# Performance work log

Measured on AMD Instinct MI355X. Metric: run time of the kernel, lower is better.

Reference implementation:

```python
import jax, jax.numpy as jnp
import numpy as np

IN_CHANNELS = 512
NUM_HEADS = 8
HEAD_CH = IN_CHANNELS // NUM_HEADS


def setup_inputs() -> dict:
    key = jax.random.key(0)
    k0, k1, k2, k3, k4 = jax.random.split(key, 5)
    B, C, H, W = 4, IN_CHANNELS, 128, 128
    x = jax.random.normal(k0, (B, C, H, W), dtype=jnp.float32)
    # 1x1 Conv2d weights == per-pixel linear layers over channels
    s_in = 1.0 / np.sqrt(C)
    Wqkv = jax.random.uniform(k1, (3 * C, C), dtype=jnp.float32, minval=-s_in, maxval=s_in)
    bqkv = jax.random.uniform(k2, (3 * C,), dtype=jnp.float32, minval=-s_in, maxval=s_in)
    Wout = jax.random.uniform(k3, (C, C), dtype=jnp.float32, minval=-s_in, maxval=s_in)
    bout = jax.random.uniform(k4, (C,), dtype=jnp.float32, minval=-s_in, maxval=s_in)
    return {"x": x, "Wqkv": Wqkv, "bqkv": bqkv, "Wout": Wout, "bout": bout}


def _axial_attention(x, Wqkv, bqkv, Wout, bout):
    B, C, H, W = x.shape
    nh, d = NUM_HEADS, HEAD_CH
    scale = 1.0 / jnp.sqrt(jnp.asarray(d, dtype=x.dtype))

    # 1x1 conv qkv projection: [B, 3C, H, W]
    qkv = jnp.einsum('bchw,oc->bohw', x, Wqkv) + bqkv[None, :, None, None]
    q, k, v = jnp.split(qkv, 3, axis=1)
    # [B, nh, d, H, W]
    q = q.reshape(B, nh, d, H, W)
    k = k.reshape(B, nh, d, H, W)
    v = v.reshape(B, nh, d, H, W)

    # Row attention: for each row h, attend across width (w over u)
    scores_row = jnp.einsum('bndhw,bndhu->bnhwu', q, k) * scale  # [B,nh,H,W,W]
    probs_row = jax.nn.softmax(scores_row, axis=-1)
    out_row = jnp.einsum('bnhwu,bndhu->bndhw', probs_row, v)  # [B,nh,d,H,W]

    # Column attention: for each column w, attend across height (h over g)
    scores_col = jnp.einsum('bndhw,bndgw->bnwhg', q, k) * scale  # [B,nh,W,H,H]
    probs_col = jax.nn.softmax(scores_col, axis=-1)
    out_col = jnp.einsum('bnwhg,bndgw->bndhw', probs_col, v)  # [B,nh,d,H,W]

    out = (out_row + out_col).reshape(B, C, H, W)
    # 1x1 conv output projection
    return jnp.einsum('bchw,oc->bohw', out, Wout) + bout[None, :, None, None]


def reference(x, Wqkv, bqkv, Wout, bout):
    return _axial_attention(x, Wqkv, bqkv, Wout, bout)
```

## Files before the change

### kernel.cpp

```cpp
#include <hip/hip_runtime.h>

#define DI __device__ __forceinline__

typedef __attribute__((ext_vector_type(4))) float f32x4;
typedef __attribute__((ext_vector_type(8))) short s16x8;
typedef __attribute__((ext_vector_type(4))) short s16x4;
typedef unsigned short u16;

#define AS_G(p) ((const __attribute__((address_space(1))) void*)(p))
#define AS_L(p) ((__attribute__((address_space(3))) void*)(p))

DI short f2bf(float f) {
  union { float f; unsigned u; } v; v.f = f;
  unsigned r = v.u + 0x7FFFu + ((v.u >> 16) & 1u);
  return (short)(r >> 16);
}
DI float bf2f(short h) {
  union { unsigned u; float f; } v; v.u = ((unsigned)(u16)h) << 16; return v.f;
}

#define MFMA(a, b, c) __builtin_amdgcn_mfma_f32_16x16x32_bf16((a), (b), (c), 0, 0, 0)

__global__ void cast_weights_kernel(const float* __restrict__ wqkv, u16* __restrict__ wqkv_bf,
                                    const float* __restrict__ wout, u16* __restrict__ wout_bf) {
  const int n1 = 1536 * 512 / 4, n2 = 512 * 512 / 4;
  for (int c = blockIdx.x * blockDim.x + threadIdx.x; c < n1 + n2; c += gridDim.x * blockDim.x) {
    const float4* src; u16* dst; int idx;
    if (c < n1) { src = (const float4*)wqkv; dst = wqkv_bf; idx = c; }
    else        { src = (const float4*)wout; dst = wout_bf; idx = c - n1; }
    float4 v = src[idx];
    s16x4 o;
    o[0] = f2bf(v.x); o[1] = f2bf(v.y); o[2] = f2bf(v.z); o[3] = f2bf(v.w);
    *(s16x4*)(dst + (long)idx * 4) = o;
  }
}

template<bool IN_F32>
__global__ __launch_bounds__(256)
void transpose_kernel(const void* __restrict__ in, u16* __restrict__ out,
                      int in_rstride, int out_rstride, long plane_in, long plane_out) {
  __shared__ __align__(16) u16 t[64][72];
  const int tid = threadIdx.x;
  const long bi = (long)blockIdx.z * plane_in;
  const long bo = (long)blockIdx.z * plane_out;
  const int r0 = blockIdx.y * 64, c0 = blockIdx.x * 64;
#pragma unroll
  for (int i = 0; i < 4; ++i) {
    int c = tid + i * 256;
    int row = c >> 4, c4 = c & 15;
    s16x4 pk;
    if (IN_F32) {
      const float4 v = *(const float4*)((const float*)in + bi + (long)(r0 + row) * in_rstride + c0 + c4 * 4);
      pk[0] = f2bf(v.x); pk[1] = f2bf(v.y); pk[2] = f2bf(v.z); pk[3] = f2bf(v.w);
    } else {
      pk = *(const s16x4*)((const u16*)in + bi + (long)(r0 + row) * in_rstride + c0 + c4 * 4);
    }
    *(s16x4*)&t[row][c4 * 4] = pk;
  }
  __syncthreads();
#pragma unroll
  for (int i = 0; i < 2; ++i) {
    int c = tid + i * 256;
    int orow = c >> 3, u = c & 7;
    s16x8 pk;
#pragma unroll
    for (int j = 0; j < 8; ++j) pk[j] = (short)t[u * 8 + j][orow];
    *(s16x8*)(out + bo + (long)(c0 + orow) * out_rstride + r0 + u * 8) = pk;
  }
}

template<int EPI>
__global__ __launch_bounds__(256, 2)
void gemm_kernel(const u16* __restrict__ A, const u16* __restrict__ B,
                 const float* __restrict__ bias,
                 u16* __restrict__ out_qk, u16* __restrict__ out_v,
                 float* __restrict__ out_f) {
  __shared__ __align__(16) u16 sAB[2][16384];
  const int tid = threadIdx.x;
  const int lane = tid & 63, wid = tid >> 6;
  const int l15 = lane & 15, g4 = lane >> 4;
  const int wr = wid >> 1, wc = wid & 1;
  const int m0 = blockIdx.y * 128, n0 = blockIdx.x * 128;
  const int z = blockIdx.z;
  const u16* Bp = B + (long)z * 8388608;

  f32x4 acc[4][4];
#pragma unroll
  for (int i = 0; i < 4; ++i)
#pragma unroll
    for (int j = 0; j < 4; ++j) { f32x4 z4 = {0.f, 0.f, 0.f, 0.f}; acc[i][j] = z4; }

  const int srow = wid * 32 + (lane >> 3);
  const int su = lane & 7;
  auto stage = [&](int kt, int buf) {
    u16* As = sAB[buf];
    u16* Bs = sAB[buf] + 8192;
#pragma unroll
    for (int i = 0; i < 4; ++i) {
      int row = srow + i * 8;
      int ksw = (su ^ (row & 7)) * 8;
      __builtin_amdgcn_global_load_lds(AS_G(A + (long)(m0 + row) * 512 + kt * 64 + ksw),
                                       AS_L(As + wid * 2048 + i * 512), 16, 0, 0);
    }
#pragma unroll
    for (int i = 0; i < 4; ++i) {
      int row = srow + i * 8;
      int ksw = (su ^ (row & 7)) * 8;
      __builtin_amdgcn_global_load_lds(AS_G(Bp + (long)(n0 + row) * 512 + kt * 64 + ksw),
                                       AS_L(Bs + wid * 2048 + i * 512), 16, 0, 0);
    }
  };

  stage(0, 0);
  __syncthreads();
  int cur = 0;
  for (int kt = 0; kt < 8; ++kt) {
    if (kt < 7) stage(kt + 1, cur ^ 1);
    const u16* As = sAB[cur];
    const u16* Bs = sAB[cur] + 8192;
#pragma unroll
    for (int ks = 0; ks < 2; ++ks) {
      s16x8 af[4], bfr[4];
#pragma unroll
      for (int mi = 0; mi < 4; ++mi) {
        int row = (wr * 4 + mi) * 16 + l15;
        af[mi] = *(const s16x8*)(As + row * 64 + (((ks * 4 + g4) ^ (row & 7)) * 8));
      }
#pragma unroll
      for (int ni = 0; ni < 4; ++ni) {
        int row = (wc * 4 + ni) * 16 + l15;
        bfr[ni] = *(const s16x8*)(Bs + row * 64 + (((ks * 4 + g4) ^ (row & 7)) * 8));
      }
#pragma unroll
      for (int mi = 0; mi < 4; ++mi)
#pragma unroll
        for (int ni = 0; ni < 4; ++ni)
          acc[mi][ni] = MFMA(af[mi], bfr[ni], acc[mi][ni]);
    }
    __syncthreads();
    cur ^= 1;
  }

  u16* tile = (u16*)sAB;
  float* tilef = (float*)sAB;

  if (EPI == 0) {
    u16* qk_b = out_qk + (long)z * 16777216;
    u16* v_b  = out_v + (long)z * 8388608;
    if (m0 < 1024) {
#pragma unroll
      for (int mi = 0; mi < 4; ++mi) {
        int ol = (wr * 4 + mi) * 16 + 4 * g4;
        int o0 = m0 + ol;
        float b0 = bias[o0], b1 = bias[o0 + 1], b2 = bias[o0 + 2], b3 = bias[o0 + 3];
#pragma unroll
        for (int ni = 0; ni < 4; ++ni) {
          int pl = (wc * 4 + ni) * 16 + l15;
          s16x4 pk;
          pk[0] = f2bf(acc[mi][ni][0] + b0);
          pk[1] = f2bf(acc[mi][ni][1] + b1);
          pk[2] = f2bf(acc[mi][ni][2] + b2);
          pk[3] = f2bf(acc[mi][ni][3] + b3);
          *(s16x4*)(tile + pl * 136 + ol) = pk;
        }
      }
      __syncthreads();
#pragma unroll
      for (int i = 0; i < 8; ++i) {
        int row = i * 16 + (tid >> 4);
        int c8 = (tid & 15) * 8;
        s16x8 vr = *(const s16x8*)(tile + row * 136 + c8);
        *(s16x8*)(qk_b + (long)(n0 + row) * 1024 + m0 + c8) = vr;
      }
    } else {
#pragma unroll
      for (int mi = 0; mi < 4; ++mi) {
        int cl = (wr * 4 + mi) * 16 + 4 * g4;
        int o0 = m0 + cl;
#pragma unroll
        for (int ni = 0; ni < 4; ++ni) {
          int pl = (wc * 4 + ni) * 16 + l15;
#pragma unroll
          for (int r = 0; r < 4; ++r)
            tile[(cl + r) * 136 + pl] = (u16)f2bf(acc[mi][ni][r] + bias[o0 + r]);
        }
      }
      __syncthreads();
#pragma unroll
      for (int i = 0; i < 8; ++i) {
        int row = i * 16 + (tid >> 4);
        int c8 = (tid & 15) * 8;
        s16x8 vr = *(const s16x8*)(tile + row * 136 + c8);
        *(s16x8*)(v_b + (long)(m0 - 1024 + row) * 16384 + n0 + c8) = vr;
      }
    }
  } else {
    float* of = out_f + (long)z * 8388608;
#pragma unroll
    for (int pass = 0; pass < 2; ++pass) {
      if (pass) __syncthreads();
#pragma unroll
      for (int mi2 = 0; mi2 < 2; ++mi2) {
        int mi = pass * 2 + mi2;
        int ol = mi2 * 16 + 4 * g4 + ((wr & 1) ? 64 : 0);
        (void)ol;
      }
      if (wr == pass) {
#pragma unroll
        for (int mi = 0; mi < 4; ++mi) {
          int ol = (wr * 4 + mi) * 16 + 4 * g4;
          int o0 = m0 + ol;
          float b0 = bias[o0], b1 = bias[o0 + 1], b2 = bias[o0 + 2], b3 = bias[o0 + 3];
          float bb[4] = {b0, b1, b2, b3};
#pragma unroll
          for (int ni = 0; ni < 4; ++ni) {
            int pl = (wc * 4 + ni) * 16 + l15;
#pragma unroll
            for (int r = 0; r < 4; ++r)
              tilef[(ol - pass * 64 + r) * 136 + pl] = acc[mi][ni][r] + bb[r];
          }
        }
      }
      __syncthreads();
#pragma unroll
      for (int i = 0; i < 8; ++i) {
        int row = i * 8 + (tid >> 5);
        int c4 = (tid & 31) * 4;
        f32x4 vr = *(const f32x4*)(tilef + row * 136 + c4);
        *(f32x4*)(of + (long)(m0 + pass * 64 + row) * 16384 + n0 + c4) = vr;
      }
    }
  }
}

template<int MODE>
__global__ __launch_bounds__(512, 2)
void attn_kernel(const u16* __restrict__ qk_t_g, const u16* __restrict__ vsrc_g,
                 u16* __restrict__ outp_g) {
  __shared__ __align__(16) u16 smem[24576];
  u16* qT = smem;
  u16* kT = smem + 8192;
  u16* vS = smem + 16384;
  u16* P  = smem;

  const int tid = threadIdx.x;
  const int lane = tid & 63, wid = tid >> 6;
  const int l15 = lane & 15, g4 = lane >> 4;
  const int b = blockIdx.x >> 10;
  const int gidx = blockIdx.x & 1023;
  const int n = gidx >> 7, pos = gidx & 127;

  const u16* qk_t = qk_t_g + (long)b * 16777216;
  const u16* vsrc = vsrc_g + (long)b * 8388608;
  u16* outp = outp_g + (long)b * 8388608;

  long q_base, q_rstride;
  if (MODE == 0) { q_base = (long)pos * 128 * 1024 + n * 64; q_rstride = 1024; }
  else           { q_base = (long)pos * 1024 + n * 64;       q_rstride = 128 * 1024; }
  const long v_base = (long)n * 64 * 16384 + (long)pos * 128;

#pragma unroll
  for (int j = 0; j < 6; ++j) {
    int t = wid + j * 8;
    if (t < 32) {
      int which = t >> 4;
      int tt = t & 15;
      int row = tt * 8 + (lane >> 3);
      int u = lane & 7;
      const u16* src = qk_t + q_base + which * 512 + (long)row * q_rstride + ((u ^ (row & 7)) * 8);
      __builtin_amdgcn_global_load_lds(AS_G(src), AS_L(smem + t * 512), 16, 0, 0);
    } else {
      int tt = t - 32;
      int row = tt * 4 + (lane >> 4);
      int u = lane & 15;
      const u16* src = vsrc + v_base + (long)row * 16384 + ((u ^ (row & 15)) * 8);
      __builtin_amdgcn_global_load_lds(AS_G(src), AS_L(smem + t * 512), 16, 0, 0);
    }
  }
  __syncthreads();

  f32x4 acc[8];
#pragma unroll
  for (int nt = 0; nt < 8; ++nt) { f32x4 zz = {0.f, 0.f, 0.f, 0.f}; acc[nt] = zz; }
  s16x8 aq[2];
  {
    int row = wid * 16 + l15;
#pragma unroll
    for (int ks = 0; ks < 2; ++ks)
      aq[ks] = *(const s16x8*)(qT + row * 64 + (((ks * 4 + g4) ^ (row & 7)) * 8));
  }
#pragma unroll
  for (int nt = 0; nt < 8; ++nt) {
    int rowk = nt * 16 + l15;
#pragma unroll
    for (int ks = 0; ks < 2; ++ks) {
      s16x8 bk = *(const s16x8*)(kT + rowk * 64 + (((ks * 4 + g4) ^ (rowk & 7)) * 8));
      acc[nt] = MFMA(aq[ks], bk, acc[nt]);
    }
  }

#pragma unroll
  for (int r = 0; r < 4; ++r) {
    float m = -1e30f;
#pragma unroll
    for (int nt = 0; nt < 8; ++nt) m = fmaxf(m, acc[nt][r]);
    m = fmaxf(m, __shfl_xor(m, 1));
    m = fmaxf(m, __shfl_xor(m, 2));
    m = fmaxf(m, __shfl_xor(m, 4));
    m = fmaxf(m, __shfl_xor(m, 8));
    float s = 0.f;
#pragma unroll
    for (int nt = 0; nt < 8; ++nt) {
      float e = __expf((acc[nt][r] - m) * 0.125f);
      acc[nt][r] = e; s += e;
    }
    s += __shfl_xor(s, 1); s += __shfl_xor(s, 2);
    s += __shfl_xor(s, 4); s += __shfl_xor(s, 8);
    float rinv = 1.0f / s;
#pragma unroll
    for (int nt = 0; nt < 8; ++nt) acc[nt][r] *= rinv;
  }
  __syncthreads();

#pragma unroll
  for (int nt = 0; nt < 8; ++nt) {
    int u = nt * 16 + l15;
#pragma unroll
    for (int r = 0; r < 4; ++r) {
      int w = wid * 16 + 4 * g4 + r;
      int ch = (u >> 3) ^ (w & 15);
      P[w * 128 + ch * 8 + (u & 7)] = (u16)f2bf(acc[nt][r]);
    }
  }
  __syncthreads();

  const int mw = wid >> 2, nw = wid & 3;
  f32x4 pacc[2][2];
#pragma unroll
  for (int mi = 0; mi < 2; ++mi)
#pragma unroll
    for (int ni = 0; ni < 2; ++ni) { f32x4 zz = {0.f, 0.f, 0.f, 0.f}; pacc[mi][ni] = zz; }
#pragma unroll
  for (int ks = 0; ks < 4; ++ks) {
    s16x8 av[2], bp[2];
#pragma unroll
    for (int mi = 0; mi < 2; ++mi) {
      int d = (mw * 2 + mi) * 16 + l15;
      av[mi] = *(const s16x8*)(vS + d * 128 + (((ks * 4 + g4) ^ (d & 15)) * 8));
    }
#pragma unroll
    for (int ni = 0; ni < 2; ++ni) {
      int w = (nw * 2 + ni) * 16 + l15;
      bp[ni] = *(const s16x8*)(P + w * 128 + (((ks * 4 + g4) ^ (w & 15)) * 8));
    }
#pragma unroll
    for (int mi = 0; mi < 2; ++mi)
#pragma unroll
      for (int ni = 0; ni < 2; ++ni)
        pacc[mi][ni] = MFMA(av[mi], bp[ni], pacc[mi][ni]);
  }

  long out_pbase, out_pstr;
  if (MODE == 0) { out_pbase = (long)pos * 128 * 512; out_pstr = 512; }
  else           { out_pbase = (long)pos * 512;       out_pstr = 128 * 512; }
#pragma unroll
  for (int mi = 0; mi < 2; ++mi) {
    int d0 = (mw * 2 + mi) * 16 + 4 * g4;
#pragma unroll
    for (int ni = 0; ni < 2; ++ni) {
      int nj = (nw * 2 + ni) * 16 + l15;
      long base = out_pbase + (long)nj * out_pstr + n * 64 + d0;
      if (MODE == 0) {
        s16x4 pk;
#pragma unroll
        for (int r = 0; r < 4; ++r) pk[r] = f2bf(pacc[mi][ni][r]);
        *(s16x4*)(outp + base) = pk;
      } else {
        s16x4 old = *(const s16x4*)(outp + base);
        s16x4 pk;
#pragma unroll
        for (int r = 0; r < 4; ++r) pk[r] = f2bf(bf2f(old[r]) + pacc[mi][ni][r]);
        *(s16x4*)(outp + base) = pk;
      }
    }
  }
}

extern "C" void kernel_launch(void* const* d_in, const int* in_sizes, int n_in,
                              void* d_out, int out_size, void* d_ws, size_t ws_size,
                              hipStream_t stream) {
  const float* x    = (const float*)d_in[0];
  const float* wqkv = (const float*)d_in[1];
  const float* bqkv = (const float*)d_in[2];
  const float* wout = (const float*)d_in[3];
  const float* bout = (const float*)d_in[4];
  float* out = (float*)d_out;

  char* ws = (char*)d_ws;
  size_t off = 0;
  auto alloc = [&](size_t bytes) { void* p = ws + off; off += (bytes + 255) & ~(size_t)255; return p; };
  u16* wqkv_bf = (u16*)alloc(1536L * 512 * 2);
  u16* wout_bf = (u16*)alloc(512L * 512 * 2);
  u16* xT      = (u16*)alloc(4L * 16384 * 512 * 2);
  u16* qk_t    = (u16*)alloc(4L * 16384 * 1024 * 2);
  u16* v_buf   = (u16*)alloc(4L * 512 * 16384 * 2);
  u16* vT      = (u16*)alloc(4L * 512 * 16384 * 2);
  u16* attn_T  = (u16*)alloc(4L * 16384 * 512 * 2);

  cast_weights_kernel<<<256, 256, 0, stream>>>(wqkv, wqkv_bf, wout, wout_bf);
  transpose_kernel<true><<<dim3(256, 8, 4), 256, 0, stream>>>(
      x, xT, 16384, 512, 512L * 16384, 16384L * 512);
  gemm_kernel<0><<<dim3(128, 12, 4), 256, 0, stream>>>(wqkv_bf, xT, bqkv, qk_t, v_buf, nullptr);
  transpose_kernel<false><<<dim3(2, 2, 2048), 256, 0, stream>>>(v_buf, vT, 128, 128, 16384, 16384);
  attn_kernel<0><<<dim3(4096), 512, 0, stream>>>(qk_t, v_buf, attn_T);
  attn_kernel<1><<<dim3(4096), 512, 0, stream>>>(qk_t, vT, attn_T);
  gemm_kernel<1><<<dim3(128, 4, 4), 256, 0, stream>>>(wout_bf, attn_T, bout, nullptr, nullptr, out);
}
```

Baseline: 387.0 us.

## Load GEMM A-operand fragments directly from global into registers, staging only B in LDS

The GEMM kernel no longer stages the weight (A) tile through shared memory. Each wave loads its MFMA A fragments straight from global memory into a double-buffered register array, prefetching the next k-tile, while B is still staged in LDS via global_load_lds. This halves LDS traffic and footprint per block, which may allow higher occupancy. The cost is more registers and uncoalesced 16-byte global loads for A that rely on cache hits, since A is shared across blocks.

```diff
diff --git a/kernel.cpp b/kernel.cpp
--- a/kernel.cpp
+++ b/kernel.cpp
@@ -75,7 +75,7 @@
                  const float* __restrict__ bias,
                  u16* __restrict__ out_qk, u16* __restrict__ out_v,
                  float* __restrict__ out_f) {
-  __shared__ __align__(16) u16 sAB[2][16384];
+  __shared__ __align__(16) u16 smem[17408];
   const int tid = threadIdx.x;
   const int lane = tid & 63, wid = tid >> 6;
   const int l15 = lane & 15, g4 = lane >> 4;
@@ -92,16 +92,8 @@
 
   const int srow = wid * 32 + (lane >> 3);
   const int su = lane & 7;
-  auto stage = [&](int kt, int buf) {
-    u16* As = sAB[buf];
-    u16* Bs = sAB[buf] + 8192;
-#pragma unroll
-    for (int i = 0; i < 4; ++i) {
-      int row = srow + i * 8;
-      int ksw = (su ^ (row & 7)) * 8;
-      __builtin_amdgcn_global_load_lds(AS_G(A + (long)(m0 + row) * 512 + kt * 64 + ksw),
-                                       AS_L(As + wid * 2048 + i * 512), 16, 0, 0);
-    }
+  auto stageB = [&](int kt, int buf) {
+    u16* Bs = smem + buf * 8192;
 #pragma unroll
     for (int i = 0; i < 4; ++i) {
       int row = srow + i * 8;
@@ -111,21 +103,34 @@
     }
   };
 
-  stage(0, 0);
+  s16x8 a_frag[2][4][2];
+
+#pragma unroll
+  for (int mi = 0; mi < 4; ++mi)
+#pragma unroll
+    for (int ks = 0; ks < 2; ++ks)
+      a_frag[0][mi][ks] = *(const s16x8*)(A + (long)(m0 + (wr * 4 + mi) * 16 + l15) * 512 +
+                                          (ks * 4 + g4) * 8);
+  stageB(0, 0);
   __syncthreads();
-  int cur = 0;
+
+#pragma unroll
   for (int kt = 0; kt < 8; ++kt) {
-    if (kt < 7) stage(kt + 1, cur ^ 1);
-    const u16* As = sAB[cur];
-    const u16* Bs = sAB[cur] + 8192;
+    const int cur = kt & 1;
+    if (kt < 7) {
+#pragma unroll
+      for (int mi = 0; mi < 4; ++mi)
+#pragma unroll
+        for (int ks = 0; ks < 2; ++ks)
+          a_frag[cur ^ 1][mi][ks] =
+              *(const s16x8*)(A + (long)(m0 + (wr * 4 + mi) * 16 + l15) * 512 +
+                              (kt + 1) * 64 + (ks * 4 + g4) * 8);
+      stageB(kt + 1, cur ^ 1);
+    }
+    const u16* Bs = smem + cur * 8192;
 #pragma unroll
     for (int ks = 0; ks < 2; ++ks) {
-      s16x8 af[4], bfr[4];
-#pragma unroll
-      for (int mi = 0; mi < 4; ++mi) {
-        int row = (wr * 4 + mi) * 16 + l15;
-        af[mi] = *(const s16x8*)(As + row * 64 + (((ks * 4 + g4) ^ (row & 7)) * 8));
-      }
+      s16x8 bfr[4];
 #pragma unroll
       for (int ni = 0; ni < 4; ++ni) {
         int row = (wc * 4 + ni) * 16 + l15;
@@ -135,14 +140,13 @@
       for (int mi = 0; mi < 4; ++mi)
 #pragma unroll
         for (int ni = 0; ni < 4; ++ni)
-          acc[mi][ni] = MFMA(af[mi], bfr[ni], acc[mi][ni]);
+          acc[mi][ni] = MFMA(a_frag[cur][mi][ks], bfr[ni], acc[mi][ni]);
     }
     __syncthreads();
-    cur ^= 1;
-  }
-
-  u16* tile = (u16*)sAB;
-  float* tilef = (float*)sAB;
+  }
+
+  u16* tile = smem;
+  float* tilef = (float*)smem;
 
   if (EPI == 0) {
     u16* qk_b = out_qk + (long)z * 16777216;
@@ -199,19 +203,12 @@
 #pragma unroll
     for (int pass = 0; pass < 2; ++pass) {
       if (pass) __syncthreads();
-#pragma unroll
-      for (int mi2 = 0; mi2 < 2; ++mi2) {
-        int mi = pass * 2 + mi2;
-        int ol = mi2 * 16 + 4 * g4 + ((wr & 1) ? 64 : 0);
-        (void)ol;
-      }
       if (wr == pass) {
 #pragma unroll
         for (int mi = 0; mi < 4; ++mi) {
           int ol = (wr * 4 + mi) * 16 + 4 * g4;
           int o0 = m0 + ol;
-          float b0 = bias[o0], b1 = bias[o0 + 1], b2 = bias[o0 + 2], b3 = bias[o0 + 3];
-          float bb[4] = {b0, b1, b2, b3};
+          float bb[4] = {bias[o0], bias[o0 + 1], bias[o0 + 2], bias[o0 + 3]};
 #pragma unroll
           for (int ni = 0; ni < 4; ++ni) {
             int pl = (wc * 4 + ni) * 16 + l15;
```

Measured after the change: 490.5 us. 26.7% more time.

## Enlarge GEMM tiles to 256x256 with 512-thread blocks

Applied to the files above, without the earlier changes.

Both projection GEMMs move from 128x128 tiles with 4 waves to 256x256 tiles with 8 waves, each wave computing a 128x64 sub-tile. Operand staging, the swizzled LDS layout and the multi-pass epilogues are rewritten to fit the larger 128KB shared buffer. The aim is more arithmetic per loaded byte and less global traffic for the A/B operands. In exchange, each block uses far more LDS and registers, which likely allows only one block per CU. The grid also shrinks to fewer blocks, so load balance across CUs may suffer.

```diff
diff --git a/kernel.cpp b/kernel.cpp
--- a/kernel.cpp
+++ b/kernel.cpp
@@ -70,163 +70,169 @@
 }
 
 template<int EPI>
-__global__ __launch_bounds__(256, 2)
+__global__ __launch_bounds__(512, 2)
 void gemm_kernel(const u16* __restrict__ A, const u16* __restrict__ B,
                  const float* __restrict__ bias,
                  u16* __restrict__ out_qk, u16* __restrict__ out_v,
                  float* __restrict__ out_f) {
-  __shared__ __align__(16) u16 sAB[2][16384];
+  __shared__ __align__(16) u16 smem[65536];
   const int tid = threadIdx.x;
   const int lane = tid & 63, wid = tid >> 6;
   const int l15 = lane & 15, g4 = lane >> 4;
-  const int wr = wid >> 1, wc = wid & 1;
-  const int m0 = blockIdx.y * 128, n0 = blockIdx.x * 128;
+  const int wr = wid >> 2, wc = wid & 3;
+  const int m0 = blockIdx.y * 256, n0 = blockIdx.x * 256;
   const int z = blockIdx.z;
   const u16* Bp = B + (long)z * 8388608;
 
-  f32x4 acc[4][4];
-#pragma unroll
-  for (int i = 0; i < 4; ++i)
+  f32x4 acc[8][4];
+#pragma unroll
+  for (int i = 0; i < 8; ++i)
 #pragma unroll
     for (int j = 0; j < 4; ++j) { f32x4 z4 = {0.f, 0.f, 0.f, 0.f}; acc[i][j] = z4; }
 
-  const int srow = wid * 32 + (lane >> 3);
-  const int su = lane & 7;
   auto stage = [&](int kt, int buf) {
-    u16* As = sAB[buf];
-    u16* Bs = sAB[buf] + 8192;
+    u16* As = smem + buf * 32768;
+    u16* Bs = As + 16384;
 #pragma unroll
     for (int i = 0; i < 4; ++i) {
-      int row = srow + i * 8;
-      int ksw = (su ^ (row & 7)) * 8;
-      __builtin_amdgcn_global_load_lds(AS_G(A + (long)(m0 + row) * 512 + kt * 64 + ksw),
-                                       AS_L(As + wid * 2048 + i * 512), 16, 0, 0);
+      int unit = tid + i * 512;
+      int row = unit >> 3;
+      int csw = ((unit & 7) ^ (row & 7)) * 8;
+      __builtin_amdgcn_global_load_lds(AS_G(A + (long)(m0 + row) * 512 + kt * 64 + csw),
+                                       AS_L(As + unit * 8), 16, 0, 0);
     }
 #pragma unroll
     for (int i = 0; i < 4; ++i) {
-      int row = srow + i * 8;
-      int ksw = (su ^ (row & 7)) * 8;
-      __builtin_amdgcn_global_load_lds(AS_G(Bp + (long)(n0 + row) * 512 + kt * 64 + ksw),
-                                       AS_L(Bs + wid * 2048 + i * 512), 16, 0, 0);
+      int unit = tid + i * 512;
+      int row = unit >> 3;
+      int csw = ((unit & 7) ^ (row & 7)) * 8;
+      __builtin_amdgcn_global_load_lds(AS_G(Bp + (long)(n0 + row) * 512 + kt * 64 + csw),
+                                       AS_L(Bs + unit * 8), 16, 0, 0);
     }
   };
 
   stage(0, 0);
   __syncthreads();
-  int cur = 0;
+#pragma unroll 2
   for (int kt = 0; kt < 8; ++kt) {
+    const int cur = kt & 1;
     if (kt < 7) stage(kt + 1, cur ^ 1);
-    const u16* As = sAB[cur];
-    const u16* Bs = sAB[cur] + 8192;
+    const u16* As = smem + cur * 32768;
+    const u16* Bs = As + 16384;
 #pragma unroll
     for (int ks = 0; ks < 2; ++ks) {
-      s16x8 af[4], bfr[4];
-#pragma unroll
-      for (int mi = 0; mi < 4; ++mi) {
-        int row = (wr * 4 + mi) * 16 + l15;
+      s16x8 af[8], bfr[4];
+#pragma unroll
+      for (int mi = 0; mi < 8; ++mi) {
+        int row = wr * 128 + mi * 16 + l15;
         af[mi] = *(const s16x8*)(As + row * 64 + (((ks * 4 + g4) ^ (row & 7)) * 8));
       }
 #pragma unroll
       for (int ni = 0; ni < 4; ++ni) {
-        int row = (wc * 4 + ni) * 16 + l15;
+        int row = wc * 64 + ni * 16 + l15;
         bfr[ni] = *(const s16x8*)(Bs + row * 64 + (((ks * 4 + g4) ^ (row & 7)) * 8));
       }
 #pragma unroll
-      for (int mi = 0; mi < 4; ++mi)
+      for (int mi = 0; mi < 8; ++mi)
 #pragma unroll
         for (int ni = 0; ni < 4; ++ni)
           acc[mi][ni] = MFMA(af[mi], bfr[ni], acc[mi][ni]);
     }
     __syncthreads();
-    cur ^= 1;
-  }
-
-  u16* tile = (u16*)sAB;
-  float* tilef = (float*)sAB;
+  }
+
+  u16* tile = smem;
+  float* tilef = (float*)smem;
 
   if (EPI == 0) {
     u16* qk_b = out_qk + (long)z * 16777216;
     u16* v_b  = out_v + (long)z * 8388608;
     if (m0 < 1024) {
 #pragma unroll
-      for (int mi = 0; mi < 4; ++mi) {
-        int ol = (wr * 4 + mi) * 16 + 4 * g4;
-        int o0 = m0 + ol;
-        float b0 = bias[o0], b1 = bias[o0 + 1], b2 = bias[o0 + 2], b3 = bias[o0 + 3];
-#pragma unroll
-        for (int ni = 0; ni < 4; ++ni) {
-          int pl = (wc * 4 + ni) * 16 + l15;
-          s16x4 pk;
-          pk[0] = f2bf(acc[mi][ni][0] + b0);
-          pk[1] = f2bf(acc[mi][ni][1] + b1);
-          pk[2] = f2bf(acc[mi][ni][2] + b2);
-          pk[3] = f2bf(acc[mi][ni][3] + b3);
-          *(s16x4*)(tile + pl * 136 + ol) = pk;
+      for (int pass = 0; pass < 2; ++pass) {
+        if (pass) __syncthreads();
+        if ((wc >> 1) == pass) {
+#pragma unroll
+          for (int mi = 0; mi < 8; ++mi) {
+            int ol = wr * 128 + mi * 16 + 4 * g4;
+            int o0 = m0 + ol;
+            float b0 = bias[o0], b1 = bias[o0 + 1], b2 = bias[o0 + 2], b3 = bias[o0 + 3];
+#pragma unroll
+            for (int ni = 0; ni < 4; ++ni) {
+              int pl = (wc & 1) * 64 + ni * 16 + l15;
+              s16x4 pk;
+              pk[0] = f2bf(acc[mi][ni][0] + b0);
+              pk[1] = f2bf(acc[mi][ni][1] + b1);
+              pk[2] = f2bf(acc[mi][ni][2] + b2);
+              pk[3] = f2bf(acc[mi][ni][3] + b3);
+              *(s16x4*)(tile + pl * 264 + ol) = pk;
+            }
+          }
         }
-      }
-      __syncthreads();
-#pragma unroll
-      for (int i = 0; i < 8; ++i) {
-        int row = i * 16 + (tid >> 4);
-        int c8 = (tid & 15) * 8;
-        s16x8 vr = *(const s16x8*)(tile + row * 136 + c8);
-        *(s16x8*)(qk_b + (long)(n0 + row) * 1024 + m0 + c8) = vr;
+        __syncthreads();
+#pragma unroll
+        for (int i = 0; i < 8; ++i) {
+          int unit = tid + i * 512;
+          int row = unit >> 5, c8 = (unit & 31) * 8;
+          s16x8 vr = *(const s16x8*)(tile + row * 264 + c8);
+          *(s16x8*)(qk_b + (long)(n0 + pass * 128 + row) * 1024 + m0 + c8) = vr;
+        }
       }
     } else {
 #pragma unroll
-      for (int mi = 0; mi < 4; ++mi) {
-        int cl = (wr * 4 + mi) * 16 + 4 * g4;
-        int o0 = m0 + cl;
-#pragma unroll
-        for (int ni = 0; ni < 4; ++ni) {
-          int pl = (wc * 4 + ni) * 16 + l15;
-#pragma unroll
-          for (int r = 0; r < 4; ++r)
-            tile[(cl + r) * 136 + pl] = (u16)f2bf(acc[mi][ni][r] + bias[o0 + r]);
+      for (int pass = 0; pass < 2; ++pass) {
+        if (pass) __syncthreads();
+        if (wr == pass) {
+#pragma unroll
+          for (int mi = 0; mi < 8; ++mi) {
+            int cll = mi * 16 + 4 * g4;
+            int o0 = m0 + wr * 128 + cll;
+#pragma unroll
+            for (int ni = 0; ni < 4; ++ni) {
+              int pl = wc * 64 + ni * 16 + l15;
+#pragma unroll
+              for (int r = 0; r < 4; ++r)
+                tile[(cll + r) * 264 + pl] = (u16)f2bf(acc[mi][ni][r] + bias[o0 + r]);
+            }
+          }
         }
-      }
-      __syncthreads();
-#pragma unroll
-      for (int i = 0; i < 8; ++i) {
-        int row = i * 16 + (tid >> 4);
-        int c8 = (tid & 15) * 8;
-        s16x8 vr = *(const s16x8*)(tile + row * 136 + c8);
-        *(s16x8*)(v_b + (long)(m0 - 1024 + row) * 16384 + n0 + c8) = vr;
+        __syncthreads();
+#pragma unroll
+        for (int i = 0; i < 8; ++i) {
+          int unit = tid + i * 512;
+          int row = unit >> 5, c8 = (unit & 31) * 8;
+          s16x8 vr = *(const s16x8*)(tile + row * 264 + c8);
+          *(s16x8*)(v_b + (long)(m0 - 1024 + pass * 128 + row) * 16384 + n0 + c8) = vr;
+        }
       }
     }
   } else {
     float* of = out_f + (long)z * 8388608;
 #pragma unroll
-    for (int pass = 0; pass < 2; ++pass) {
+    for (int pass = 0; pass < 4; ++pass) {
       if (pass) __syncthreads();
-#pragma unroll
-      for (int mi2 = 0; mi2 < 2; ++mi2) {
-        int mi = pass * 2 + mi2;
-        int ol = mi2 * 16 + 4 * g4 + ((wr & 1) ? 64 : 0);
-        (void)ol;
-      }
-      if (wr == pass) {
-#pragma unroll
-        for (int mi = 0; mi < 4; ++mi) {
-          int ol = (wr * 4 + mi) * 16 + 4 * g4;
-          int o0 = m0 + ol;
-          float b0 = bias[o0], b1 = bias[o0 + 1], b2 = bias[o0 + 2], b3 = bias[o0 + 3];
-          float bb[4] = {b0, b1, b2, b3};
+      if (wr == (pass >> 1)) {
+#pragma unroll
+        for (int mi2 = 0; mi2 < 4; ++mi2) {
+          int mi = (pass & 1) * 4 + mi2;
+          int oll = mi2 * 16 + 4 * g4;
+          int o0 = m0 + wr * 128 + mi * 16 + 4 * g4;
+          float bb[4] = {bias[o0], bias[o0 + 1], bias[o0 + 2], bias[o0 + 3]};
 #pragma unroll
           for (int ni = 0; ni < 4; ++ni) {
-            int pl = (wc * 4 + ni) * 16 + l15;
+            int pl = wc * 64 + ni * 16 + l15;
 #pragma unroll
             for (int r = 0; r < 4; ++r)
-              tilef[(ol - pass * 64 + r) * 136 + pl] = acc[mi][ni][r] + bb[r];
+              tilef[(oll + r) * 264 + pl] = acc[mi][ni][r] + bb[r];
           }
         }
       }
       __syncthreads();
 #pragma unroll
       for (int i = 0; i < 8; ++i) {
-        int row = i * 8 + (tid >> 5);
-        int c4 = (tid & 31) * 4;
-        f32x4 vr = *(const f32x4*)(tilef + row * 136 + c4);
+        int unit = tid + i * 512;
+        int row = unit >> 6, c4 = (unit & 63) * 4;
+        f32x4 vr = *(const f32x4*)(tilef + row * 264 + c4);
         *(f32x4*)(of + (long)(m0 + pass * 64 + row) * 16384 + n0 + c4) = vr;
       }
     }
@@ -410,9 +416,9 @@
   cast_weights_kernel<<<256, 256, 0, stream>>>(wqkv, wqkv_bf, wout, wout_bf);
   transpose_kernel<true><<<dim3(256, 8, 4), 256, 0, stream>>>(
       x, xT, 16384, 512, 512L * 16384, 16384L * 512);
-  gemm_kernel<0><<<dim3(128, 12, 4), 256, 0, stream>>>(wqkv_bf, xT, bqkv, qk_t, v_buf, nullptr);
+  gemm_kernel<0><<<dim3(64, 6, 4), 512, 0, stream>>>(wqkv_bf, xT, bqkv, qk_t, v_buf, nullptr);
   transpose_kernel<false><<<dim3(2, 2, 2048), 256, 0, stream>>>(v_buf, vT, 128, 128, 16384, 16384);
   attn_kernel<0><<<dim3(4096), 512, 0, stream>>>(qk_t, v_buf, attn_T);
   attn_kernel<1><<<dim3(4096), 512, 0, stream>>>(qk_t, vT, attn_T);
-  gemm_kernel<1><<<dim3(128, 4, 4), 256, 0, stream>>>(wout_bf, attn_T, bout, nullptr, nullptr, out);
-}
+  gemm_kernel<1><<<dim3(64, 2, 4), 512, 0, stream>>>(wout_bf, attn_T, bout, nullptr, nullptr, out);
+}
```

Measured after the change: 392.5 us. About the same (+1.4%).

## Stage attention output through LDS, split load waits, raise MFMA priority

Applied to the files above, without the earlier changes.

The attention kernel now issues Q/K loads and V loads in separate groups and waits only on the Q/K loads (vmcnt(2)) before computing scores. This lets the V fetch overlap with the QK^T MFMAs and softmax. Wave priority is raised around both MFMA loops. The output tile is transposed through shared memory in fp32, so each row of 64 channels is written contiguously by 16 threads instead of scattered 8-byte stores. The extra barriers and the LDS round-trip add latency, and the partial vmcnt wait relies on the exact ordering of the load instructions.

```diff
diff --git a/kernel.cpp b/kernel.cpp
--- a/kernel.cpp
+++ b/kernel.cpp
@@ -199,19 +199,12 @@
 #pragma unroll
     for (int pass = 0; pass < 2; ++pass) {
       if (pass) __syncthreads();
-#pragma unroll
-      for (int mi2 = 0; mi2 < 2; ++mi2) {
-        int mi = pass * 2 + mi2;
-        int ol = mi2 * 16 + 4 * g4 + ((wr & 1) ? 64 : 0);
-        (void)ol;
-      }
       if (wr == pass) {
 #pragma unroll
         for (int mi = 0; mi < 4; ++mi) {
           int ol = (wr * 4 + mi) * 16 + 4 * g4;
           int o0 = m0 + ol;
-          float b0 = bias[o0], b1 = bias[o0 + 1], b2 = bias[o0 + 2], b3 = bias[o0 + 3];
-          float bb[4] = {b0, b1, b2, b3};
+          float bb[4] = {bias[o0], bias[o0 + 1], bias[o0 + 2], bias[o0 + 3]};
 #pragma unroll
           for (int ni = 0; ni < 4; ++ni) {
             int pl = (wc * 4 + ni) * 16 + l15;
@@ -242,6 +235,7 @@
   u16* kT = smem + 8192;
   u16* vS = smem + 16384;
   u16* P  = smem;
+  float* Tf = (float*)smem;
 
   const int tid = threadIdx.x;
   const int lane = tid & 63, wid = tid >> 6;
@@ -260,24 +254,26 @@
   const long v_base = (long)n * 64 * 16384 + (long)pos * 128;
 
 #pragma unroll
-  for (int j = 0; j < 6; ++j) {
-    int t = wid + j * 8;
-    if (t < 32) {
-      int which = t >> 4;
-      int tt = t & 15;
-      int row = tt * 8 + (lane >> 3);
-      int u = lane & 7;
-      const u16* src = qk_t + q_base + which * 512 + (long)row * q_rstride + ((u ^ (row & 7)) * 8);
-      __builtin_amdgcn_global_load_lds(AS_G(src), AS_L(smem + t * 512), 16, 0, 0);
-    } else {
-      int tt = t - 32;
-      int row = tt * 4 + (lane >> 4);
-      int u = lane & 15;
-      const u16* src = vsrc + v_base + (long)row * 16384 + ((u ^ (row & 15)) * 8);
-      __builtin_amdgcn_global_load_lds(AS_G(src), AS_L(smem + t * 512), 16, 0, 0);
-    }
-  }
-  __syncthreads();
+  for (int j = 0; j < 4; ++j) {
+    int t = wid * 4 + j;
+    int which = t >> 4;
+    int tt = t & 15;
+    int row = tt * 8 + (lane >> 3);
+    int u = lane & 7;
+    const u16* src = qk_t + q_base + which * 512 + (long)row * q_rstride + ((u ^ (row & 7)) * 8);
+    __builtin_amdgcn_global_load_lds(AS_G(src), AS_L(smem + t * 512), 16, 0, 0);
+  }
+#pragma unroll
+  for (int j = 0; j < 2; ++j) {
+    int tt = wid * 2 + j;
+    int row = tt * 4 + (lane >> 4);
+    int u = lane & 15;
+    const u16* src = vsrc + v_base + (long)row * 16384 + ((u ^ (row & 15)) * 8);
+    __builtin_amdgcn_global_load_lds(AS_G(src), AS_L(smem + (32 + tt) * 512), 16, 0, 0);
+  }
+  asm volatile("s_waitcnt vmcnt(2)" ::: "memory");
+  __builtin_amdgcn_s_barrier();
+  __builtin_amdgcn_sched_barrier(0);
 
   f32x4 acc[8];
 #pragma unroll
@@ -289,6 +285,7 @@
     for (int ks = 0; ks < 2; ++ks)
       aq[ks] = *(const s16x8*)(qT + row * 64 + (((ks * 4 + g4) ^ (row & 7)) * 8));
   }
+  __builtin_amdgcn_s_setprio(1);
 #pragma unroll
   for (int nt = 0; nt < 8; ++nt) {
     int rowk = nt * 16 + l15;
@@ -298,6 +295,7 @@
       acc[nt] = MFMA(aq[ks], bk, acc[nt]);
     }
   }
+  __builtin_amdgcn_s_setprio(0);
 
 #pragma unroll
   for (int r = 0; r < 4; ++r) {
@@ -340,6 +338,7 @@
   for (int mi = 0; mi < 2; ++mi)
 #pragma unroll
     for (int ni = 0; ni < 2; ++ni) { f32x4 zz = {0.f, 0.f, 0.f, 0.f}; pacc[mi][ni] = zz; }
+  __builtin_amdgcn_s_setprio(1);
 #pragma unroll
   for (int ks = 0; ks < 4; ++ks) {
     s16x8 av[2], bp[2];
@@ -359,30 +358,36 @@
       for (int ni = 0; ni < 2; ++ni)
         pacc[mi][ni] = MFMA(av[mi], bp[ni], pacc[mi][ni]);
   }
-
-  long out_pbase, out_pstr;
-  if (MODE == 0) { out_pbase = (long)pos * 128 * 512; out_pstr = 512; }
-  else           { out_pbase = (long)pos * 512;       out_pstr = 128 * 512; }
+  __builtin_amdgcn_s_setprio(0);
+  __syncthreads();
+
 #pragma unroll
   for (int mi = 0; mi < 2; ++mi) {
     int d0 = (mw * 2 + mi) * 16 + 4 * g4;
 #pragma unroll
     for (int ni = 0; ni < 2; ++ni) {
       int nj = (nw * 2 + ni) * 16 + l15;
-      long base = out_pbase + (long)nj * out_pstr + n * 64 + d0;
-      if (MODE == 0) {
-        s16x4 pk;
-#pragma unroll
-        for (int r = 0; r < 4; ++r) pk[r] = f2bf(pacc[mi][ni][r]);
-        *(s16x4*)(outp + base) = pk;
-      } else {
-        s16x4 old = *(const s16x4*)(outp + base);
-        s16x4 pk;
-#pragma unroll
-        for (int r = 0; r < 4; ++r) pk[r] = f2bf(bf2f(old[r]) + pacc[mi][ni][r]);
-        *(s16x4*)(outp + base) = pk;
-      }
-    }
+      *(f32x4*)(Tf + nj * 68 + d0) = pacc[mi][ni];
+    }
+  }
+  __syncthreads();
+#pragma unroll
+  for (int i = 0; i < 4; ++i) {
+    int row = (tid >> 4) + i * 32;
+    int c4 = (tid & 15) * 4;
+    f32x4 v4 = *(const f32x4*)(Tf + row * 68 + c4);
+    long p = (MODE == 0) ? ((long)pos * 128 + row) : ((long)row * 128 + pos);
+    u16* dst = outp + p * 512 + n * 64 + c4;
+    s16x4 pk;
+    if (MODE == 0) {
+#pragma unroll
+      for (int r = 0; r < 4; ++r) pk[r] = f2bf(v4[r]);
+    } else {
+      s16x4 old = *(const s16x4*)dst;
+#pragma unroll
+      for (int r = 0; r < 4; ++r) pk[r] = f2bf(bf2f(old[r]) + v4[r]);
+    }
+    *(s16x4*)dst = pk;
   }
 }
 
```

Result: faster. 378.3 us, median of 3 (-2.3%).
